# Kernel optimization log

Measured on AMD Instinct MI355X. Metric: run time of the kernel, lower is better.

## Reference

```python
import jax, jax.numpy as jnp
import numpy as np

N_NODES, IN_DIM, HID, LAT, N_EDGES = 50000, 3000, 512, 30, 800000
NEG_SLOPE = 0.2


def setup_inputs() -> dict:
    key = jax.random.key(0)
    ks = jax.random.split(key, 6)
    x = jax.random.normal(ks[0], (N_NODES, IN_DIM), dtype=jnp.float32)
    edge_index = jax.random.randint(ks[1], (2, N_EDGES), 0, N_NODES, dtype=jnp.int64)
    # xavier-normal-ish scales
    W1 = jax.random.normal(ks[2], (IN_DIM, HID), dtype=jnp.float32) * 0.02
    W2 = jax.random.normal(ks[3], (HID, LAT), dtype=jnp.float32) * 0.06
    att_src = jax.random.normal(ks[4], (HID,), dtype=jnp.float32) * 0.1
    att_dst = jax.random.normal(ks[5], (HID,), dtype=jnp.float32) * 0.1
    return {"x": x, "edge_index": edge_index, "W1": W1, "W2": W2,
            "att_src": att_src, "att_dst": att_dst}


def _segment_softmax(e, seg, num_segments):
    # numerically stable softmax over variable-degree dst neighborhoods
    m = jax.ops.segment_max(e, seg, num_segments=num_segments)
    m = jnp.where(jnp.isfinite(m), m, 0.0)  # empty segments -> 0, harmless
    p = jnp.exp(e - m[seg])
    s = jax.ops.segment_sum(p, seg, num_segments=num_segments)
    return p / (s[seg] + 1e-16)


def reference(x, edge_index, W1, W2, att_src, att_dst):
    N = x.shape[0]
    src, dst = edge_index[0], edge_index[1]  # messages flow src(j) -> dst(i)

    # ---- conv1: full GAT layer (heads=1, no self-loops, no bias) ----
    h1 = x @ W1                                   # [N, 512]
    a_src = h1 @ att_src                          # [N]
    a_dst = h1 @ att_dst                          # [N]
    e = jax.nn.leaky_relu(a_src[src] + a_dst[dst], NEG_SLOPE)  # [E]
    alpha = _segment_softmax(e, dst, N)           # [E] (also tied attn for conv3)
    agg1 = jax.ops.segment_sum(h1[src] * alpha[:, None], dst, num_segments=N)
    x1 = jax.nn.elu(agg1)                         # [N, 512]

    # ---- conv2: attention=False -> plain linear projection ----
    x2 = x1 @ W2                                  # [N, 30] (latent embedding)

    # ---- conv3: tied weights (W2^T) + tied attention from conv1 ----
    h3 = x2 @ W2.T                                # [N, 512]
    agg3 = jax.ops.segment_sum(h3[src] * alpha[:, None], dst, num_segments=N)
    x3 = jax.nn.elu(agg3)

    # ---- conv4: attention=False, tied weights (W1^T) ----
    x4 = x3 @ W1.T                                # [N, in_channels]
    return (x2, x4)
```

## Files before the change

### kernel.cpp

```cpp
#include <hip/hip_runtime.h>

#define N_NODES 50000
#define IN_DIM  3000
#define HID     512
#define LAT     30
#define N_EDGES 800000
#define M_PAD   50048
#define M_PAD2  50176
#define K1_PAD  3008
#define N4_PAD  3072

typedef __bf16 bf16;
typedef unsigned int uint;
typedef __attribute__((ext_vector_type(4))) float f32x4;
typedef __attribute__((ext_vector_type(8))) bf16 bf16x8;

__device__ __forceinline__ float bf2f(bf16 b){ return (float)b; }

__device__ __forceinline__ void gl16(const void* g, void* l){
  __builtin_amdgcn_global_load_lds(
      (const __attribute__((address_space(1))) void*)g,
      (__attribute__((address_space(3))) void*)l, 16, 0, 0);
}

__device__ __forceinline__ int xcd_swz(int orig, int nwg){
  int q = nwg >> 3, r = nwg & 7;
  int xcd = orig & 7, lid = orig >> 3;
  return (xcd < r ? xcd*(q+1) : r*(q+1) + (xcd-r)*q) + lid;
}

__global__ void k_w1t(const float* __restrict__ W1, bf16* __restrict__ W1T){
  int k = blockIdx.x*256 + threadIdx.x;
  int n = blockIdx.y;
  if (k >= K1_PAD) return;
  float v = (k < IN_DIM) ? W1[(long)k*HID + n] : 0.f;
  int kt = k >> 5, c = (k >> 3) & 3, off = k & 7;
  int p = c ^ ((n >> 1) & 3);
  W1T[(long)n*K1_PAD + kt*32 + p*8 + off] = (bf16)v;
}
__global__ void k_w1p(const float* __restrict__ W1, bf16* __restrict__ W1P){
  int k = blockIdx.x*256 + threadIdx.x;
  int n = blockIdx.y;
  if (k >= HID) return;
  float v = (n < IN_DIM) ? W1[(long)n*HID + k] : 0.f;
  int kt = k >> 5, c = (k >> 3) & 3, off = k & 7;
  int p = c ^ ((n >> 1) & 3);
  W1P[(long)n*HID + kt*32 + p*8 + off] = (bf16)v;
}
__global__ void k_w2t(const float* __restrict__ W2, bf16* __restrict__ W2T){
  int k = blockIdx.x*256 + threadIdx.x;
  int n = blockIdx.y;
  if (k >= HID) return;
  float v = (n < LAT) ? W2[(long)k*LAT + n] : 0.f;
  W2T[(long)n*HID + k] = (bf16)v;
}
__global__ void k_w2p(const float* __restrict__ W2, bf16* __restrict__ W2P){
  int t = blockIdx.x*256 + threadIdx.x;
  if (t >= HID*32) return;
  int n = t >> 5, k = t & 31;
  W2P[t] = (bf16)((k < LAT) ? W2[(long)n*LAT + k] : 0.f);
}

__global__ __launch_bounds__(256) void k_cvt(const float* __restrict__ x, bf16* __restrict__ xb){
  int chunk = blockIdx.x*256 + threadIdx.x;
  int row = blockIdx.y;
  if (chunk >= K1_PAD/8) return;
  int c8 = chunk*8;
  bf16x8 o;
  if (row < N_NODES && c8 + 8 <= IN_DIM){
    float4 v0 = *(const float4*)(x + (long)row*IN_DIM + c8);
    float4 v1 = *(const float4*)(x + (long)row*IN_DIM + c8 + 4);
    o[0]=(bf16)v0.x; o[1]=(bf16)v0.y; o[2]=(bf16)v0.z; o[3]=(bf16)v0.w;
    o[4]=(bf16)v1.x; o[5]=(bf16)v1.y; o[6]=(bf16)v1.z; o[7]=(bf16)v1.w;
  } else {
    #pragma unroll
    for (int j=0;j<8;j++){
      int c = c8 + j;
      float v = (row < N_NODES && c < IN_DIM) ? x[(long)row*IN_DIM + c] : 0.f;
      o[j] = (bf16)v;
    }
  }
  *(bf16x8*)(xb + (long)row*K1_PAD + c8) = o;
}

template<bool C_F32>
__global__ __launch_bounds__(512, 2) void gemm2(
    const bf16* __restrict__ A, const bf16* __restrict__ B, void* __restrict__ Cp,
    int lda, int ldb, int KS, int Mvalid, int Nvalid, int ldc, int NBX)
{
  __shared__ bf16 Alds[2][256*32];
  __shared__ bf16 Blds[2][256*32];
  const int tid  = threadIdx.x;
  const int lane = tid & 63;
  const int w    = tid >> 6;
  const int wm   = (w >> 2) * 128;
  const int wn   = (w & 3) * 64;
  const int wgid = xcd_swz(blockIdx.x, gridDim.x);
  const int col0 = (wgid % NBX) * 256, row0 = (wgid / NBX) * 256;

  f32x4 acc[8][4];
  #pragma unroll
  for (int mi=0;mi<8;mi++)
    #pragma unroll
    for (int ni=0;ni<4;ni++)
      acc[mi][ni] = (f32x4){0.f,0.f,0.f,0.f};

  const int srow = tid >> 2;
  const int acl  = (((tid & 3) ^ ((tid >> 3) & 3))) * 8;
  const long a0 = (long)(row0 +       srow) * lda;
  const long a1 = (long)(row0 + 128 + srow) * lda;
  const long b0 = (long)(col0 +       srow) * ldb + (tid & 3) * 8;
  const long b1 = (long)(col0 + 128 + srow) * ldb + (tid & 3) * 8;

#define STG2(buf, ks) do{                                               \
    const int kb_ = (ks) * 32;                                          \
    char* la_ = (char*)&Alds[buf][0] + tid*16;                          \
    char* lb_ = (char*)&Blds[buf][0] + tid*16;                          \
    gl16(A + a0 + kb_ + acl, la_);                                      \
    gl16(A + a1 + kb_ + acl, la_ + 8192);                               \
    gl16(B + b0 + kb_, lb_);                                            \
    gl16(B + b1 + kb_, lb_ + 8192);                                     \
  }while(0)

  STG2(0, 0);

  const int rl = lane & 15;
  const int g  = lane >> 4;
  const int ph = (g ^ ((rl >> 1) & 3)) * 16;

  for (int ks = 0; ks < KS; ks++){
    const int cur = ks & 1;
    if (ks + 1 < KS){
      STG2(cur^1, ks+1);
      asm volatile("s_waitcnt vmcnt(4)" ::: "memory");
    } else {
      asm volatile("s_waitcnt vmcnt(0)" ::: "memory");
    }
    __builtin_amdgcn_s_barrier();

    const char* Ac = (const char*)&Alds[cur][0] + (wm + rl)*64 + ph;
    const char* Bc = (const char*)&Blds[cur][0] + (wn + rl)*64 + ph;
    bf16x8 afr[8], bfr[4];
    #pragma unroll
    for (int mi=0;mi<8;mi++) afr[mi] = *(const bf16x8*)(Ac + mi*1024);
    #pragma unroll
    for (int ni=0;ni<4;ni++) bfr[ni] = *(const bf16x8*)(Bc + ni*1024);
    #pragma unroll
    for (int mi=0;mi<8;mi++)
      #pragma unroll
      for (int ni=0;ni<4;ni++)
        acc[mi][ni] = __builtin_amdgcn_mfma_f32_16x16x32_bf16(afr[mi], bfr[ni], acc[mi][ni], 0, 0, 0);

    __builtin_amdgcn_s_barrier();
  }
#undef STG2

  const int crb  = (lane >> 4) * 4;
  const int ccol = lane & 15;
  #pragma unroll
  for (int mi=0;mi<8;mi++){
    #pragma unroll
    for (int v=0;v<4;v++){
      int r = row0 + wm + mi*16 + crb + v;
      if (r >= Mvalid) continue;
      #pragma unroll
      for (int ni=0;ni<4;ni++){
        int c = col0 + wn + ni*16 + ccol;
        if (c >= Nvalid) continue;
        float val = acc[mi][ni][v];
        if (C_F32) ((float*)Cp)[(long)r*ldc + c] = val;
        else       ((bf16*)Cp)[(long)r*ldc + c] = (bf16)val;
      }
    }
  }
}

template<bool C_F32, bool ELU>
__global__ __launch_bounds__(256) void gemm_glds(
    const bf16* __restrict__ A, const bf16* __restrict__ B, void* __restrict__ Cp,
    int lda, int ldb, int Ksteps, int Mvalid, int Nvalid, int ldc, int NBX)
{
  __shared__ bf16 Alds[2][128*32];
  __shared__ bf16 Blds[2][128*32];
  const int tid  = threadIdx.x;
  const int lane = tid & 63;
  const int w    = tid >> 6;
  const int wm   = (w >> 1) * 64, wn = (w & 1) * 64;
  const int wgid = xcd_swz(blockIdx.x, gridDim.x);
  const int col0 = (wgid % NBX) * 128, row0 = (wgid / NBX) * 128;

  f32x4 acc[4][4];
  #pragma unroll
  for (int mi=0;mi<4;mi++)
    #pragma unroll
    for (int ni=0;ni<4;ni++)
      acc[mi][ni] = (f32x4){0.f,0.f,0.f,0.f};

  const int sr = tid >> 2;
  const int sc = (tid & 3) * 16;
  const char* ga = (const char*)(A + (long)(row0 + sr) * lda) + sc;
  const char* gb = (const char*)(B + (long)(col0 + sr) * ldb) + sc;
  const long astep = (long)64 * lda * 2;
  const long bstep = (long)64 * ldb * 2;

#define STAGE_G(buf, ks) do{                                            \
    const long ko_ = (long)(ks) * 64;                                   \
    char* la_ = (char*)&Alds[buf][0] + sr*64 + sc;                      \
    char* lb_ = (char*)&Blds[buf][0] + sr*64 + sc;                      \
    gl16(ga + ko_,         la_);                                        \
    gl16(ga + ko_ + astep, la_ + 64*64);                                \
    gl16(gb + ko_,         lb_);                                        \
    gl16(gb + ko_ + bstep, lb_ + 64*64);                                \
  }while(0)

  STAGE_G(0, 0);

  for (int ks = 0; ks < Ksteps; ks++){
    const int cur = ks & 1;
    if (ks + 1 < Ksteps){
      STAGE_G(cur^1, ks+1);
      asm volatile("s_waitcnt vmcnt(4)" ::: "memory");
    } else {
      asm volatile("s_waitcnt vmcnt(0)" ::: "memory");
    }
    __builtin_amdgcn_s_barrier();

    const bf16* Ac = &Alds[cur][0];
    const bf16* Bc = &Blds[cur][0];
    bf16x8 af[4], bfr[4];
    #pragma unroll
    for (int mi=0;mi<4;mi++)
      af[mi] = *(const bf16x8*)&Ac[(wm + mi*16 + (lane & 15))*32 + (lane>>4)*8];
    #pragma unroll
    for (int ni=0;ni<4;ni++)
      bfr[ni] = *(const bf16x8*)&Bc[(wn + ni*16 + (lane & 15))*32 + (lane>>4)*8];
    #pragma unroll
    for (int mi=0;mi<4;mi++)
      #pragma unroll
      for (int ni=0;ni<4;ni++)
        acc[mi][ni] = __builtin_amdgcn_mfma_f32_16x16x32_bf16(af[mi], bfr[ni], acc[mi][ni], 0, 0, 0);

    __builtin_amdgcn_s_barrier();
  }
#undef STAGE_G

  const int crb  = (lane >> 4) * 4;
  const int ccol = lane & 15;
  #pragma unroll
  for (int mi=0;mi<4;mi++){
    #pragma unroll
    for (int v=0;v<4;v++){
      int r = row0 + wm + mi*16 + crb + v;
      if (r >= Mvalid) continue;
      #pragma unroll
      for (int ni=0;ni<4;ni++){
        int c = col0 + wn + ni*16 + ccol;
        if (c >= Nvalid) continue;
        float val = acc[mi][ni][v];
        if (ELU) val = (val > 0.f) ? val : expm1f(val);
        if (C_F32) ((float*)Cp)[(long)r*ldc + c] = val;
        else       ((bf16*)Cp)[(long)r*ldc + c] = (bf16)val;
      }
    }
  }
}

__global__ void k_attdots(const bf16* __restrict__ h1, const float* __restrict__ att_s,
                          const float* __restrict__ att_d, float* __restrict__ a_src,
                          float* __restrict__ a_dst){
  int gid = blockIdx.x * blockDim.x + threadIdx.x;
  int row = gid >> 6, lane = gid & 63;
  if (row >= N_NODES) return;
  bf16x8 hv = *(const bf16x8*)(h1 + (long)row*HID + lane*8);
  float s1 = 0.f, s2 = 0.f;
  #pragma unroll
  for (int j=0;j<8;j++){
    float h = bf2f(hv[j]);
    s1 = fmaf(h, att_s[lane*8+j], s1);
    s2 = fmaf(h, att_d[lane*8+j], s2);
  }
  #pragma unroll
  for (int o=32;o>0;o>>=1){ s1 += __shfl_down(s1,o); s2 += __shfl_down(s2,o); }
  if (lane == 0){ a_src[row] = s1; a_dst[row] = s2; }
}

__global__ void k_deg(const int* __restrict__ ei, int* __restrict__ deg){
  int e = blockIdx.x*256 + threadIdx.x;
  if (e >= N_EDGES) return;
  atomicAdd(&deg[ei[N_EDGES + e]], 1);
}

__global__ void k_scan(const int* __restrict__ deg, int* __restrict__ off, int* __restrict__ cur){
  const int n = M_PAD, T = 1024;
  int t = threadIdx.x;
  const int per = (n + T - 1) / T;
  int s0 = t*per, s1 = min(n, s0+per);
  int sum = 0;
  for (int i=s0;i<s1;i++) sum += deg[i];
  __shared__ int sd[1024];
  sd[t] = sum; __syncthreads();
  for (int o=1;o<T;o<<=1){
    int x = (t>=o) ? sd[t-o] : 0;
    __syncthreads();
    sd[t] += x;
    __syncthreads();
  }
  int run = sd[t] - sum;
  for (int i=s0;i<s1;i++){
    off[i] = run; cur[i] = run;
    run += deg[i];
  }
  if (s0 < n && s1 == n) off[n] = run;
}

__global__ void k_fill(const int* __restrict__ ei, int* __restrict__ cur,
                       int* __restrict__ csr_src, const float* __restrict__ a_s,
                       const float* __restrict__ a_d, float* __restrict__ p_e){
  int e = blockIdx.x*256 + threadIdx.x;
  if (e >= N_EDGES) return;
  int s = ei[e];
  int d = ei[N_EDGES + e];
  int pos = atomicAdd(&cur[d], 1);
  csr_src[pos] = s;
  float v = a_s[s] + a_d[d];
  v = (v > 0.f) ? v : 0.2f*v;
  p_e[pos] = __expf(v);
}

__global__ __launch_bounds__(256) void k_agg1w(
    const int* __restrict__ off, const int* __restrict__ csr_src,
    const float* __restrict__ p_edge,
    const bf16* __restrict__ h1, bf16* __restrict__ x1,
    float* __restrict__ s_node)
{
  const int i = blockIdx.x*4 + (threadIdx.x >> 6);
  const int lane = threadIdx.x & 63;
  if (i >= N_NODES) return;
  const int start = off[i];
  const int deg = off[i+1] - start;

  float acc[8];
  #pragma unroll
  for (int j=0;j<8;j++) acc[j] = 0.f;
  float ssum = 0.f;

  for (int k=0;k<deg;k++){
    int s = csr_src[start+k];
    float pk = p_edge[start+k];
    ssum += pk;
    bf16x8 hv = *(const bf16x8*)(h1 + (long)s*HID + lane*8);
    #pragma unroll
    for (int j=0;j<8;j++) acc[j] = fmaf(pk, bf2f(hv[j]), acc[j]);
  }
  float inv = 1.f/(ssum + 1e-16f);
  bf16x8 o;
  #pragma unroll
  for (int j=0;j<8;j++){
    float v = acc[j]*inv;
    v = (v > 0.f) ? v : expm1f(v);
    o[j] = (bf16)v;
  }
  *(bf16x8*)(x1 + (long)i*HID + lane*8) = o;
  if (lane == 0) s_node[i] = ssum;
}

__global__ void k_agg3(const int* __restrict__ off, const int* __restrict__ csr_src,
                       const float* __restrict__ p_edge, const float* __restrict__ s_node,
                       const float* __restrict__ x2, bf16* __restrict__ aggb)
{
  int i = blockIdx.x*8 + (threadIdx.x >> 5);
  int lane = threadIdx.x & 31;
  if (i >= M_PAD2) return;
  float acc = 0.f;
  if (i < N_NODES){
    int s0 = off[i], d = off[i+1] - s0;
    for (int k=0;k<d;k++){
      int s = csr_src[s0+k];
      float pk = p_edge[s0+k];
      if (lane < LAT) acc = fmaf(pk, x2[(long)s*LAT + lane], acc);
    }
    acc *= 1.f/(s_node[i] + 1e-16f);
  }
  aggb[(long)i*32 + lane] = (bf16)((lane < LAT) ? acc : 0.f);
}

extern "C" void kernel_launch(void* const* d_in, const int* in_sizes, int n_in,
                              void* d_out, int out_size, void* d_ws, size_t ws_size,
                              hipStream_t stream)
{
  const float* x     = (const float*)d_in[0];
  const int*   ei    = (const int*)d_in[1];
  const float* W1    = (const float*)d_in[2];
  const float* W2    = (const float*)d_in[3];
  const float* att_s = (const float*)d_in[4];
  const float* att_d = (const float*)d_in[5];

  float* out_x2 = (float*)d_out;
  float* out_x4 = (float*)d_out + (long)N_NODES*LAT;

  bf16* xb = (bf16*)out_x4;
  bf16* h1 = xb + (long)M_PAD2*K1_PAD;
  bf16* x1 = h1 + (long)M_PAD*HID;

  char* w = (char*)d_ws;
  bf16* W1T = (bf16*)w;  w += (long)HID*K1_PAD*2;
  bf16* W1P = (bf16*)w;  w += (long)N4_PAD*HID*2;
  bf16* W2T = (bf16*)w;  w += (long)128*HID*2;
  bf16* W2P = (bf16*)w;  w += (long)HID*32*2;
  bf16* x3  = (bf16*)w;  w += (long)M_PAD2*HID*2;
  bf16* aggb= (bf16*)w;  w += (long)M_PAD2*32*2;
  int* deg  = (int*)w;   w += (long)M_PAD*4;
  int* offs = (int*)w;   w += (long)(M_PAD+64)*4;
  int* cur  = (int*)w;   w += (long)M_PAD*4;
  int* csr  = (int*)w;   w += (long)N_EDGES*4;
  float* p_e = (float*)w; w += (long)N_EDGES*4;
  float* s_n = (float*)w; w += (long)M_PAD*4;
  float* a_s = (float*)w; w += (long)M_PAD*4;
  float* a_d = (float*)w; w += (long)M_PAD*4;

  k_w1t<<<dim3((K1_PAD+255)/256, HID), 256, 0, stream>>>(W1, W1T);
  k_w1p<<<dim3((HID+255)/256, N4_PAD), 256, 0, stream>>>(W1, W1P);
  k_w2t<<<dim3(2, 128), 256, 0, stream>>>(W2, W2T);
  k_w2p<<<(HID*32+255)/256, 256, 0, stream>>>(W2, W2P);
  k_cvt<<<dim3((K1_PAD/8+255)/256, M_PAD2), 256, 0, stream>>>(x, xb);

  hipMemsetAsync(deg, 0, (size_t)M_PAD*4, stream);
  k_deg<<<(N_EDGES+255)/256, 256, 0, stream>>>(ei, deg);
  k_scan<<<1, 1024, 0, stream>>>(deg, offs, cur);

  gemm2<false><<<(HID/256)*(M_PAD2/256), 512, 0, stream>>>(
      xb, W1T, h1, K1_PAD, K1_PAD, K1_PAD/32, N_NODES, HID, HID, HID/256);

  k_attdots<<<(N_NODES*64)/256, 256, 0, stream>>>(h1, att_s, att_d, a_s, a_d);

  k_fill<<<(N_EDGES+255)/256, 256, 0, stream>>>(ei, cur, csr, a_s, a_d, p_e);

  k_agg1w<<<(N_NODES+3)/4, 256, 0, stream>>>(offs, csr, p_e, h1, x1, s_n);

  gemm_glds<true,false><<<1*(M_PAD/128), 256, 0, stream>>>(
      x1, W2T, out_x2, HID, HID, HID/32, N_NODES, LAT, LAT, 1);

  k_agg3<<<(M_PAD2+7)/8, 256, 0, stream>>>(offs, csr, p_e, s_n, out_x2, aggb);
  gemm_glds<false,true><<<(HID/128)*(M_PAD2/128), 256, 0, stream>>>(
      aggb, W2P, x3, 32, 32, 1, M_PAD2, HID, HID, HID/128);

  gemm2<true><<<(N4_PAD/256)*(M_PAD2/256), 512, 0, stream>>>(
      x3, W1P, out_x4, HID, HID, HID/32, N_NODES, IN_DIM, IN_DIM, N4_PAD/256);
}
```

Baseline: 1.190 ms.

## Use 128x128 glds GEMM for first projection, simplify convert, unroll aggregation

The first projection (x @ W1) now runs on the 128x128-tile global-load-to-LDS GEMM instead of the 256x256 tile kernel. W1T is therefore stored in plain layout rather than the XOR-swizzled layout. The bf16 conversion kernel uses one block per real row and no longer writes the padded rows. The conv1 aggregation loop is unrolled by two so two neighbor rows are gathered at once. The smaller GEMM tile rereads the A matrix more often and may have more LDS bank conflicts, while the unroll aims to expose more memory-level parallelism in the gather.

```diff
diff --git a/kernel.cpp b/kernel.cpp
--- a/kernel.cpp
+++ b/kernel.cpp
@@ -34,9 +34,7 @@
   int n = blockIdx.y;
   if (k >= K1_PAD) return;
   float v = (k < IN_DIM) ? W1[(long)k*HID + n] : 0.f;
-  int kt = k >> 5, c = (k >> 3) & 3, off = k & 7;
-  int p = c ^ ((n >> 1) & 3);
-  W1T[(long)n*K1_PAD + kt*32 + p*8 + off] = (bf16)v;
+  W1T[(long)n*K1_PAD + k] = (bf16)v;
 }
 __global__ void k_w1p(const float* __restrict__ W1, bf16* __restrict__ W1P){
   int k = blockIdx.x*256 + threadIdx.x;
@@ -61,26 +59,112 @@
   W2P[t] = (bf16)((k < LAT) ? W2[(long)n*LAT + k] : 0.f);
 }
 
-__global__ __launch_bounds__(256) void k_cvt(const float* __restrict__ x, bf16* __restrict__ xb){
-  int chunk = blockIdx.x*256 + threadIdx.x;
-  int row = blockIdx.y;
+__global__ __launch_bounds__(384) void k_cvt(const float* __restrict__ x, bf16* __restrict__ xb){
+  int chunk = threadIdx.x;
+  int row = blockIdx.x;
   if (chunk >= K1_PAD/8) return;
   int c8 = chunk*8;
   bf16x8 o;
-  if (row < N_NODES && c8 + 8 <= IN_DIM){
+  if (c8 + 8 <= IN_DIM){
     float4 v0 = *(const float4*)(x + (long)row*IN_DIM + c8);
     float4 v1 = *(const float4*)(x + (long)row*IN_DIM + c8 + 4);
     o[0]=(bf16)v0.x; o[1]=(bf16)v0.y; o[2]=(bf16)v0.z; o[3]=(bf16)v0.w;
     o[4]=(bf16)v1.x; o[5]=(bf16)v1.y; o[6]=(bf16)v1.z; o[7]=(bf16)v1.w;
   } else {
     #pragma unroll
-    for (int j=0;j<8;j++){
-      int c = c8 + j;
-      float v = (row < N_NODES && c < IN_DIM) ? x[(long)row*IN_DIM + c] : 0.f;
-      o[j] = (bf16)v;
-    }
+    for (int j=0;j<8;j++) o[j] = (bf16)0.f;
   }
   *(bf16x8*)(xb + (long)row*K1_PAD + c8) = o;
+}
+
+template<bool C_F32, bool ELU>
+__global__ __launch_bounds__(256) void gemm_glds(
+    const bf16* __restrict__ A, const bf16* __restrict__ B, void* __restrict__ Cp,
+    int lda, int ldb, int Ksteps, int Mvalid, int Nvalid, int ldc, int NBX)
+{
+  __shared__ bf16 Alds[2][128*32];
+  __shared__ bf16 Blds[2][128*32];
+  const int tid  = threadIdx.x;
+  const int lane = tid & 63;
+  const int w    = tid >> 6;
+  const int wm   = (w >> 1) * 64, wn = (w & 1) * 64;
+  const int wgid = xcd_swz(blockIdx.x, gridDim.x);
+  const int col0 = (wgid % NBX) * 128, row0 = (wgid / NBX) * 128;
+
+  f32x4 acc[4][4];
+  #pragma unroll
+  for (int mi=0;mi<4;mi++)
+    #pragma unroll
+    for (int ni=0;ni<4;ni++)
+      acc[mi][ni] = (f32x4){0.f,0.f,0.f,0.f};
+
+  const int sr = tid >> 2;
+  const int sc = (tid & 3) * 16;
+  const char* ga = (const char*)(A + (long)(row0 + sr) * lda) + sc;
+  const char* gb = (const char*)(B + (long)(col0 + sr) * ldb) + sc;
+  const long astep = (long)64 * lda * 2;
+  const long bstep = (long)64 * ldb * 2;
+
+#define STAGE_G(buf, ks) do{                                            \
+    const long ko_ = (long)(ks) * 64;                                   \
+    char* la_ = (char*)&Alds[buf][0] + sr*64 + sc;                      \
+    char* lb_ = (char*)&Blds[buf][0] + sr*64 + sc;                      \
+    gl16(ga + ko_,         la_);                                        \
+    gl16(ga + ko_ + astep, la_ + 64*64);                                \
+    gl16(gb + ko_,         lb_);                                        \
+    gl16(gb + ko_ + bstep, lb_ + 64*64);                                \
+  }while(0)
+
+  STAGE_G(0, 0);
+
+  for (int ks = 0; ks < Ksteps; ks++){
+    const int cur = ks & 1;
+    if (ks + 1 < Ksteps){
+      STAGE_G(cur^1, ks+1);
+      asm volatile("s_waitcnt vmcnt(4)" ::: "memory");
+    } else {
+      asm volatile("s_waitcnt vmcnt(0)" ::: "memory");
+    }
+    __builtin_amdgcn_s_barrier();
+
+    const bf16* Ac = &Alds[cur][0];
+    const bf16* Bc = &Blds[cur][0];
+    bf16x8 af[4], bfr[4];
+    #pragma unroll
+    for (int mi=0;mi<4;mi++)
+      af[mi] = *(const bf16x8*)&Ac[(wm + mi*16 + (lane & 15))*32 + (lane>>4)*8];
+    #pragma unroll
+    for (int ni=0;ni<4;ni++)
+      bfr[ni] = *(const bf16x8*)&Bc[(wn + ni*16 + (lane & 15))*32 + (lane>>4)*8];
+    #pragma unroll
+    for (int mi=0;mi<4;mi++)
+      #pragma unroll
+      for (int ni=0;ni<4;ni++)
+        acc[mi][ni] = __builtin_amdgcn_mfma_f32_16x16x32_bf16(af[mi], bfr[ni], acc[mi][ni], 0, 0, 0);
+
+    __builtin_amdgcn_s_barrier();
+  }
+#undef STAGE_G
+
+  const int crb  = (lane >> 4) * 4;
+  const int ccol = lane & 15;
+  #pragma unroll
+  for (int mi=0;mi<4;mi++){
+    #pragma unroll
+    for (int v=0;v<4;v++){
+      int r = row0 + wm + mi*16 + crb + v;
+      if (r >= Mvalid) continue;
+      #pragma unroll
+      for (int ni=0;ni<4;ni++){
+        int c = col0 + wn + ni*16 + ccol;
+        if (c >= Nvalid) continue;
+        float val = acc[mi][ni][v];
+        if (ELU) val = (val > 0.f) ? val : expm1f(val);
+        if (C_F32) ((float*)Cp)[(long)r*ldc + c] = val;
+        else       ((bf16*)Cp)[(long)r*ldc + c] = (bf16)val;
+      }
+    }
+  }
 }
 
 template<bool C_F32>
@@ -175,96 +259,6 @@
   }
 }
 
-template<bool C_F32, bool ELU>
-__global__ __launch_bounds__(256) void gemm_glds(
-    const bf16* __restrict__ A, const bf16* __restrict__ B, void* __restrict__ Cp,
-    int lda, int ldb, int Ksteps, int Mvalid, int Nvalid, int ldc, int NBX)
-{
-  __shared__ bf16 Alds[2][128*32];
-  __shared__ bf16 Blds[2][128*32];
-  const int tid  = threadIdx.x;
-  const int lane = tid & 63;
-  const int w    = tid >> 6;
-  const int wm   = (w >> 1) * 64, wn = (w & 1) * 64;
-  const int wgid = xcd_swz(blockIdx.x, gridDim.x);
-  const int col0 = (wgid % NBX) * 128, row0 = (wgid / NBX) * 128;
-
-  f32x4 acc[4][4];
-  #pragma unroll
-  for (int mi=0;mi<4;mi++)
-    #pragma unroll
-    for (int ni=0;ni<4;ni++)
-      acc[mi][ni] = (f32x4){0.f,0.f,0.f,0.f};
-
-  const int sr = tid >> 2;
-  const int sc = (tid & 3) * 16;
-  const char* ga = (const char*)(A + (long)(row0 + sr) * lda) + sc;
-  const char* gb = (const char*)(B + (long)(col0 + sr) * ldb) + sc;
-  const long astep = (long)64 * lda * 2;
-  const long bstep = (long)64 * ldb * 2;
-
-#define STAGE_G(buf, ks) do{                                            \
-    const long ko_ = (long)(ks) * 64;                                   \
-    char* la_ = (char*)&Alds[buf][0] + sr*64 + sc;                      \
-    char* lb_ = (char*)&Blds[buf][0] + sr*64 + sc;                      \
-    gl16(ga + ko_,         la_);                                        \
-    gl16(ga + ko_ + astep, la_ + 64*64);                                \
-    gl16(gb + ko_,         lb_);                                        \
-    gl16(gb + ko_ + bstep, lb_ + 64*64);                                \
-  }while(0)
-
-  STAGE_G(0, 0);
-
-  for (int ks = 0; ks < Ksteps; ks++){
-    const int cur = ks & 1;
-    if (ks + 1 < Ksteps){
-      STAGE_G(cur^1, ks+1);
-      asm volatile("s_waitcnt vmcnt(4)" ::: "memory");
-    } else {
-      asm volatile("s_waitcnt vmcnt(0)" ::: "memory");
-    }
-    __builtin_amdgcn_s_barrier();
-
-    const bf16* Ac = &Alds[cur][0];
-    const bf16* Bc = &Blds[cur][0];
-    bf16x8 af[4], bfr[4];
-    #pragma unroll
-    for (int mi=0;mi<4;mi++)
-      af[mi] = *(const bf16x8*)&Ac[(wm + mi*16 + (lane & 15))*32 + (lane>>4)*8];
-    #pragma unroll
-    for (int ni=0;ni<4;ni++)
-      bfr[ni] = *(const bf16x8*)&Bc[(wn + ni*16 + (lane & 15))*32 + (lane>>4)*8];
-    #pragma unroll
-    for (int mi=0;mi<4;mi++)
-      #pragma unroll
-      for (int ni=0;ni<4;ni++)
-        acc[mi][ni] = __builtin_amdgcn_mfma_f32_16x16x32_bf16(af[mi], bfr[ni], acc[mi][ni], 0, 0, 0);
-
-    __builtin_amdgcn_s_barrier();
-  }
-#undef STAGE_G
-
-  const int crb  = (lane >> 4) * 4;
-  const int ccol = lane & 15;
-  #pragma unroll
-  for (int mi=0;mi<4;mi++){
-    #pragma unroll
-    for (int v=0;v<4;v++){
-      int r = row0 + wm + mi*16 + crb + v;
-      if (r >= Mvalid) continue;
-      #pragma unroll
-      for (int ni=0;ni<4;ni++){
-        int c = col0 + wn + ni*16 + ccol;
-        if (c >= Nvalid) continue;
-        float val = acc[mi][ni][v];
-        if (ELU) val = (val > 0.f) ? val : expm1f(val);
-        if (C_F32) ((float*)Cp)[(long)r*ldc + c] = val;
-        else       ((bf16*)Cp)[(long)r*ldc + c] = (bf16)val;
-      }
-    }
-  }
-}
-
 __global__ void k_attdots(const bf16* __restrict__ h1, const float* __restrict__ att_s,
                           const float* __restrict__ att_d, float* __restrict__ a_src,
                           float* __restrict__ a_dst){
@@ -344,7 +338,20 @@
   for (int j=0;j<8;j++) acc[j] = 0.f;
   float ssum = 0.f;
 
-  for (int k=0;k<deg;k++){
+  int k = 0;
+  for (; k+1 < deg; k += 2){
+    int s0 = csr_src[start+k],   s1 = csr_src[start+k+1];
+    float p0 = p_edge[start+k],  p1 = p_edge[start+k+1];
+    ssum += p0 + p1;
+    bf16x8 h0 = *(const bf16x8*)(h1 + (long)s0*HID + lane*8);
+    bf16x8 hv1 = *(const bf16x8*)(h1 + (long)s1*HID + lane*8);
+    #pragma unroll
+    for (int j=0;j<8;j++){
+      acc[j] = fmaf(p0, bf2f(h0[j]), acc[j]);
+      acc[j] = fmaf(p1, bf2f(hv1[j]), acc[j]);
+    }
+  }
+  if (k < deg){
     int s = csr_src[start+k];
     float pk = p_edge[start+k];
     ssum += pk;
@@ -399,7 +406,7 @@
   float* out_x4 = (float*)d_out + (long)N_NODES*LAT;
 
   bf16* xb = (bf16*)out_x4;
-  bf16* h1 = xb + (long)M_PAD2*K1_PAD;
+  bf16* h1 = xb + (long)M_PAD*K1_PAD;
   bf16* x1 = h1 + (long)M_PAD*HID;
 
   char* w = (char*)d_ws;
@@ -422,14 +429,14 @@
   k_w1p<<<dim3((HID+255)/256, N4_PAD), 256, 0, stream>>>(W1, W1P);
   k_w2t<<<dim3(2, 128), 256, 0, stream>>>(W2, W2T);
   k_w2p<<<(HID*32+255)/256, 256, 0, stream>>>(W2, W2P);
-  k_cvt<<<dim3((K1_PAD/8+255)/256, M_PAD2), 256, 0, stream>>>(x, xb);
+  k_cvt<<<N_NODES, 384, 0, stream>>>(x, xb);
 
   hipMemsetAsync(deg, 0, (size_t)M_PAD*4, stream);
   k_deg<<<(N_EDGES+255)/256, 256, 0, stream>>>(ei, deg);
   k_scan<<<1, 1024, 0, stream>>>(deg, offs, cur);
 
-  gemm2<false><<<(HID/256)*(M_PAD2/256), 512, 0, stream>>>(
-      xb, W1T, h1, K1_PAD, K1_PAD, K1_PAD/32, N_NODES, HID, HID, HID/256);
+  gemm_glds<false,false><<<(HID/128)*(M_PAD/128), 256, 0, stream>>>(
+      xb, W1T, h1, K1_PAD, K1_PAD, K1_PAD/32, N_NODES, HID, HID, HID/128);
 
   k_attdots<<<(N_NODES*64)/256, 256, 0, stream>>>(h1, att_s, att_d, a_s, a_d);
 
```

New measurement: 1.155 ms. -2.9%, faster.
